# Optimization experiments

Hardware: AMD Instinct MI355X
Metric: run time of the kernel (lower is better)

## Reference

```python
import jax, jax.numpy as jnp
import numpy as np

N_NODES = 50000
BN_EPS = 1e-5


def setup_inputs() -> dict:
    key = jax.random.key(0)
    ks = jax.random.split(key, 16)
    N, IN, H, OUT, E = N_NODES, 512, 128, 64, 800000
    s = lambda fi, fo: 1.0 / np.sqrt(fi)
    inp = {
        'x': jax.random.normal(ks[0], (N, IN), dtype=jnp.float32),
        'edge_index': jax.random.randint(ks[1], (2, E), 0, N, dtype=jnp.int32),
        # mlpA: Linear(N -> H)
        'WA': jax.random.uniform(ks[2], (H, N), jnp.float32, -s(N, H), s(N, H)),
        'bA': jax.random.uniform(ks[3], (H,), jnp.float32, -s(N, H), s(N, H)),
        # mlpX: Linear(IN -> H)
        'WX': jax.random.uniform(ks[4], (H, IN), jnp.float32, -s(IN, H), s(IN, H)),
        'bX': jax.random.uniform(ks[5], (H,), jnp.float32, -s(IN, H), s(IN, H)),
        # W: Linear(2H -> H)
        'W': jax.random.uniform(ks[6], (H, 2 * H), jnp.float32, -s(2 * H, H), s(2 * H, H)),
        'bW': jax.random.uniform(ks[7], (H,), jnp.float32, -s(2 * H, H), s(2 * H, H)),
        # mlp_final layer 1: Linear(H -> H) + BN
        'Wf1': jax.random.uniform(ks[8], (H, H), jnp.float32, -s(H, H), s(H, H)),
        'bf1': jax.random.uniform(ks[9], (H,), jnp.float32, -s(H, H), s(H, H)),
        'gamma': jnp.ones((H,), jnp.float32),
        'beta': jnp.zeros((H,), jnp.float32),
        # mlp_final layer 2: Linear(H -> OUT)
        'Wf2': jax.random.uniform(ks[10], (OUT, H), jnp.float32, -s(H, OUT), s(H, OUT)),
        'bf2': jax.random.uniform(ks[11], (OUT,), jnp.float32, -s(H, OUT), s(H, OUT)),
    }
    return inp


def _batchnorm(x, gamma, beta):
    # training-mode BN over the node/batch axis (biased variance, as in torch)
    mean = jnp.mean(x, axis=0)
    var = jnp.var(x, axis=0)
    return (x - mean) * jax.lax.rsqrt(var + BN_EPS) * gamma + beta


def reference(x, edge_index, WA, bA, WX, bX, W, bW, Wf1, bf1, gamma, beta, Wf2, bf2):
    row, col = edge_index[0], edge_index[1]
    row = row - row.min()
    # xA = A @ WA.T + bA  where A[i,j]=1 per (row,col) edge (duplicates sum).
    # Equivalent SpMM: gather columns of WA at `col`, segment-sum into `row`.
    xA = jax.ops.segment_sum(WA.T[col], row, num_segments=N_NODES) + bA  # [N, H]
    xX = x @ WX.T + bX  # [N, H]
    h = jnp.concatenate([xA, xX], axis=-1) @ W.T + bW  # [N, H]
    h = jax.nn.relu(h + xA + xX)
    # mlp_final (num_layers=2): Linear -> ReLU -> BN -> (dropout off) -> Linear
    h = jax.nn.relu(h @ Wf1.T + bf1)
    h = _batchnorm(h, gamma, beta)
    out = h @ Wf2.T + bf2  # [N, OUT]
    return out
```

## Files before the change

### kernel.cpp

```cpp
#include <hip/hip_runtime.h>

typedef __bf16 bf16_t;
typedef __bf16 bf16x8 __attribute__((ext_vector_type(8)));
typedef float f32x4 __attribute__((ext_vector_type(4)));

#define IN_DIM 512
#define H_DIM 128
#define OUT_DIM 64
#define BN_EPS 1e-5f
#define SCAN_BLK 2048

#define MFMA(a, b, c) __builtin_amdgcn_mfma_f32_16x16x32_bf16(a, b, c, 0, 0, 0)

__device__ __forceinline__ float ld_adapt(const void* p, size_t i, int isbf) {
    return isbf ? (float)((const bf16_t*)p)[i] : ((const float*)p)[i];
}

__device__ __forceinline__ void split8(const float* p, bf16x8& hi, bf16x8& lo) {
    f32x4 v0 = *(const f32x4*)p;
    f32x4 v1 = *(const f32x4*)(p + 4);
#pragma unroll
    for (int i = 0; i < 8; ++i) {
        float f = (i < 4) ? v0[i] : v1[i - 4];
        bf16_t h = (bf16_t)f;
        hi[i] = h;
        lo[i] = (bf16_t)(f - (float)h);
    }
}

__device__ __forceinline__ void loadAraw(const void* x, size_t elemoff, int isbf,
                                         f32x4& p0, f32x4& p1) {
    if (isbf) {
        p0 = *(const f32x4*)((const bf16_t*)x + elemoff);
    } else {
        const float* fp = (const float*)x + elemoff;
        p0 = *(const f32x4*)fp;
        p1 = *(const f32x4*)(fp + 4);
    }
}

__device__ __forceinline__ void cvtA(const f32x4& p0, const f32x4& p1, int isbf,
                                     bf16x8& ah, bf16x8& al) {
    if (isbf) {
        ah = __builtin_bit_cast(bf16x8, p0);
#pragma unroll
        for (int i = 0; i < 8; ++i) al[i] = (bf16_t)0.f;
    } else {
#pragma unroll
        for (int i = 0; i < 8; ++i) {
            float f = (i < 4) ? p0[i] : p1[i - 4];
            bf16_t h = (bf16_t)f;
            ah[i] = h;
            al[i] = (bf16_t)(f - (float)h);
        }
    }
}

__global__ void k_init(const void* bA, const void* bX, const void* bW, const void* bf1,
                       const void* gamma, const void* beta, const void* bf2,
                       float* __restrict__ dst, int* __restrict__ flag) {
    __shared__ int s_isbf;
    if (threadIdx.x == 0) {
        unsigned u = *(const unsigned*)gamma;
        int f = (u == 0x3F803F80u) ? 1 : 0;
        *flag = f;
        s_isbf = f;
    }
    __syncthreads();
    int isbf = s_isbf;
    int t = threadIdx.x;
    dst[t] = ld_adapt(bA, t, isbf);
    dst[128 + t] = ld_adapt(bX, t, isbf);
    dst[256 + t] = ld_adapt(bW, t, isbf);
    dst[384 + t] = ld_adapt(bf1, t, isbf);
    dst[512 + t] = ld_adapt(gamma, t, isbf);
    dst[640 + t] = ld_adapt(beta, t, isbf);
    if (t < OUT_DIM) dst[768 + t] = ld_adapt(bf2, t, isbf);
}

__global__ __launch_bounds__(256) void k_transpose(const void* __restrict__ WA,
                                                   float* __restrict__ WAT, int N,
                                                   const int* __restrict__ flag) {
    __shared__ float t[64][130];
    int isbf = *flag;
    int n0 = blockIdx.x * 64;
    int tid = threadIdx.x;
#pragma unroll
    for (int i = 0; i < 32; ++i) {
        int lin = i * 256 + tid;
        int h = lin >> 6, nl = lin & 63;
        int n = n0 + nl;
        t[nl][h] = (n < N) ? ld_adapt(WA, (size_t)h * N + n, isbf) : 0.f;
    }
    __syncthreads();
#pragma unroll
    for (int i = 0; i < 32; ++i) {
        int lin = i * 256 + tid;
        int nl = lin >> 7, h = lin & 127;
        int n = n0 + nl;
        if (n < N) WAT[(size_t)n * H_DIM + h] = t[nl][h];
    }
}

__global__ __launch_bounds__(256) void k_prep(const int* __restrict__ rows, int E,
                                              int* __restrict__ bmin, int* __restrict__ cnt) {
    __shared__ int sm[4];
    int i = blockIdx.x * 256 + threadIdx.x;
    int m = 0x7fffffff;
    if (i < E) {
        int r = rows[i];
        m = r;
        atomicAdd(&cnt[r], 1);
    }
    for (int off = 32; off; off >>= 1) m = min(m, __shfl_xor(m, off, 64));
    if ((threadIdx.x & 63) == 0) sm[threadIdx.x >> 6] = m;
    __syncthreads();
    if (threadIdx.x == 0)
        bmin[blockIdx.x] = min(min(sm[0], sm[1]), min(sm[2], sm[3]));
}

__global__ __launch_bounds__(256) void k_scan1(const int* __restrict__ cnt,
                                               int* __restrict__ offs,
                                               int* __restrict__ bsum, int N) {
    __shared__ int ts[256];
    int base = blockIdx.x * SCAN_BLK;
    int t = threadIdx.x;
    int v[8], s = 0;
#pragma unroll
    for (int i = 0; i < 8; ++i) {
        int idx = base + t * 8 + i;
        v[i] = (idx < N) ? cnt[idx] : 0;
        s += v[i];
    }
    ts[t] = s;
    __syncthreads();
    for (int off = 1; off < 256; off <<= 1) {
        int x = (t >= off) ? ts[t - off] : 0;
        __syncthreads();
        ts[t] += x;
        __syncthreads();
    }
    int run = ts[t] - s;
#pragma unroll
    for (int i = 0; i < 8; ++i) {
        int idx = base + t * 8 + i;
        if (idx < N) offs[idx] = run;
        run += v[i];
    }
    if (t == 255) bsum[blockIdx.x] = ts[255];
}

__global__ __launch_bounds__(256) void k_scan2(int* __restrict__ bsum, int* __restrict__ offs,
                                               int NB, int N, const int* __restrict__ bmin,
                                               int nbmin, int* __restrict__ minbuf) {
    __shared__ int sm[256];
    int t = threadIdx.x;
    int m = 0x7fffffff;
    for (int i = t; i < nbmin; i += 256) m = min(m, bmin[i]);
    sm[t] = m;
    __syncthreads();
    for (int off = 128; off; off >>= 1) {
        if (t < off) sm[t] = min(sm[t], sm[t + off]);
        __syncthreads();
    }
    if (t == 0) {
        *minbuf = sm[0];
        int run = 0;
        for (int b = 0; b < NB; ++b) {
            int v = bsum[b];
            bsum[b] = run;
            run += v;
        }
        offs[N] = run;
    }
}

__global__ __launch_bounds__(256) void k_scan3(int* __restrict__ offs, const int* __restrict__ bsum,
                                               int* __restrict__ cursor, int N) {
    int i = blockIdx.x * 256 + threadIdx.x;
    if (i >= N) return;
    int v = offs[i] + bsum[i / SCAN_BLK];
    offs[i] = v;
    cursor[i] = v;
}

__global__ __launch_bounds__(256) void k_build(const int* __restrict__ rows,
                                               const int* __restrict__ cols, int E,
                                               int* __restrict__ cursor,
                                               int* __restrict__ scol) {
    int i = blockIdx.x * 256 + threadIdx.x;
    if (i >= E) return;
    int r = rows[i];
    int pos = atomicAdd(&cursor[r], 1);
    scol[pos] = cols[i];
}

__global__ __launch_bounds__(256) void k_gather(const int* __restrict__ offs,
                                                const int* __restrict__ scol,
                                                const float* __restrict__ WAT,
                                                const float* __restrict__ bA_f,
                                                const int* __restrict__ minbuf,
                                                float* __restrict__ xA, int N) {
    int wave = threadIdx.x >> 6, lane = threadIdx.x & 63;
    int r = blockIdx.x * 4 + wave;
    if (r >= N) return;
    int b = r + *minbuf;
    int s = 0, e = 0;
    if (b < N) {
        s = offs[b];
        e = offs[b + 1];
    }
    float2 a0 = {0.f, 0.f}, a1 = {0.f, 0.f}, a2 = {0.f, 0.f}, a3 = {0.f, 0.f};
    int i = s;
    for (; i + 7 < e; i += 8) {
        float2 w[8];
#pragma unroll
        for (int j = 0; j < 8; ++j) {
            int c = scol[i + j];
            w[j] = *(const float2*)(WAT + (size_t)c * H_DIM + lane * 2);
        }
        a0.x += w[0].x + w[4].x; a0.y += w[0].y + w[4].y;
        a1.x += w[1].x + w[5].x; a1.y += w[1].y + w[5].y;
        a2.x += w[2].x + w[6].x; a2.y += w[2].y + w[6].y;
        a3.x += w[3].x + w[7].x; a3.y += w[3].y + w[7].y;
    }
    for (; i + 1 < e; i += 2) {
        int c0 = scol[i], c1 = scol[i + 1];
        float2 w0 = *(const float2*)(WAT + (size_t)c0 * H_DIM + lane * 2);
        float2 w1 = *(const float2*)(WAT + (size_t)c1 * H_DIM + lane * 2);
        a0.x += w0.x; a0.y += w0.y;
        a1.x += w1.x; a1.y += w1.y;
    }
    if (i < e) {
        int c = scol[i];
        float2 w = *(const float2*)(WAT + (size_t)c * H_DIM + lane * 2);
        a2.x += w.x; a2.y += w.y;
    }
    float2 bias = *(const float2*)(bA_f + lane * 2);
    float2 out = {a0.x + a1.x + a2.x + a3.x + bias.x, a0.y + a1.y + a2.y + a3.y + bias.y};
    *(float2*)(xA + (size_t)r * H_DIM + lane * 2) = out;
}

__device__ __forceinline__ void pack_frag(const void* __restrict__ W, bf16_t* __restrict__ hi,
                                          bf16_t* __restrict__ lo, int K, int NC,
                                          int addres, int isbf, int f, int lane) {
    int ks = f / (NC >> 4), nt = f % (NC >> 4);
    int n = nt * 16 + (lane & 15);
    int k0 = ks * 32 + (lane >> 4) * 8;
    bf16_t* dh = hi + (size_t)f * 512 + lane * 8;
    bf16_t* dl = lo + (size_t)f * 512 + lane * 8;
#pragma unroll
    for (int j = 0; j < 8; ++j) {
        int kk = k0 + j;
        float v = ld_adapt(W, (size_t)n * K + kk, isbf);
        if (addres && (kk == n || kk == n + H_DIM)) v += 1.f;
        bf16_t h = (bf16_t)v;
        dh[j] = h;
        dl[j] = (bf16_t)(v - (float)h);
    }
}

__global__ __launch_bounds__(256) void k_pack3(const void* WX, bf16_t* WXh, bf16_t* WXl,
                                               const void* W, bf16_t* Wh, bf16_t* Wl,
                                               const void* Wf1, bf16_t* Wf1h, bf16_t* Wf1l,
                                               const int* __restrict__ flag) {
    int g = blockIdx.x * 256 + threadIdx.x;
    int f = g >> 6, lane = g & 63;
    int isbf = *flag;
    if (f < 128)
        pack_frag(WX, WXh, WXl, IN_DIM, H_DIM, 0, isbf, f, lane);
    else if (f < 192)
        pack_frag(W, Wh, Wl, 2 * H_DIM, H_DIM, 1, isbf, f - 128, lane);
    else if (f < 224)
        pack_frag(Wf1, Wf1h, Wf1l, H_DIM, H_DIM, 0, isbf, f - 192, lane);
}

__global__ __launch_bounds__(256, 2) void k_fuseA(
    const void* __restrict__ x, const float* __restrict__ xAf,
    const bf16_t* __restrict__ WXh, const bf16_t* __restrict__ WXl,
    const bf16_t* __restrict__ Wh, const bf16_t* __restrict__ Wl,
    const bf16_t* __restrict__ Wf1h, const bf16_t* __restrict__ Wf1l,
    const float* __restrict__ smallf, float* __restrict__ h2,
    double* __restrict__ sums, double* __restrict__ sumsq,
    const int* __restrict__ flag, int M) {
    __shared__ float ax[32 * 132];
    __shared__ float ls_sum[H_DIM], ls_sq[H_DIM];
    int tid = threadIdx.x;
    int wave = tid >> 6, lane = tid & 63, l16 = lane & 15, quad = lane >> 4;
    int band = wave & 1, half = wave >> 1;
    int ntb = half * 4;
    int mbase = blockIdx.x * 32 + band * 16;
    int isbf = *flag;
    int r0 = min(mbase + l16, M - 1);
    const float* bX = smallf + 128;
    const float* bW = smallf + 256;
    const float* bf1 = smallf + 384;

    if (tid < H_DIM) {
        ls_sum[tid] = 0.f;
        ls_sq[tid] = 0.f;
    }

    auto loadB = [&](const bf16_t* __restrict__ H, const bf16_t* __restrict__ L, int fb,
                     bf16x8 bh[4], bf16x8 bl[4]) {
        const bf16_t* hp = H + (size_t)fb * 512 + lane * 8;
        const bf16_t* lp = L + (size_t)fb * 512 + lane * 8;
#pragma unroll
        for (int nt = 0; nt < 4; ++nt) {
            bh[nt] = *(const bf16x8*)(hp + nt * 512);
            bl[nt] = *(const bf16x8*)(lp + nt * 512);
        }
    };

    f32x4 acc[4];
    bf16x8 bh[2][4], bl[2][4];
    f32x4 pa[2][2];

#pragma unroll
    for (int nt = 0; nt < 4; ++nt) acc[nt] = f32x4{0.f, 0.f, 0.f, 0.f};
    {
        size_t offx = (size_t)r0 * IN_DIM + quad * 8;
        loadAraw(x, offx, isbf, pa[0][0], pa[0][1]);
        loadB(WXh, WXl, ntb, bh[0], bl[0]);
#pragma unroll
        for (int ks = 0; ks < 16; ++ks) {
            int cur = ks & 1, nxt = cur ^ 1;
            if (ks < 15) {
                loadAraw(x, offx + (ks + 1) * 32, isbf, pa[nxt][0], pa[nxt][1]);
                loadB(WXh, WXl, (ks + 1) * 8 + ntb, bh[nxt], bl[nxt]);
            }
            bf16x8 ah, al;
            cvtA(pa[cur][0], pa[cur][1], isbf, ah, al);
#pragma unroll
            for (int nt = 0; nt < 4; ++nt) {
                acc[nt] = MFMA(ah, bh[cur][nt], acc[nt]);
                acc[nt] = MFMA(ah, bl[cur][nt], acc[nt]);
                acc[nt] = MFMA(al, bh[cur][nt], acc[nt]);
            }
        }
    }
#pragma unroll
    for (int nt = 0; nt < 4; ++nt) {
        int col = (ntb + nt) * 16 + l16;
        float b = bX[col];
#pragma unroll
        for (int r = 0; r < 4; ++r) {
            int lr = band * 16 + quad * 4 + r;
            ax[lr * 132 + col] = acc[nt][r] + b;
        }
    }
    __syncthreads();

#pragma unroll
    for (int nt = 0; nt < 4; ++nt) acc[nt] = f32x4{0.f, 0.f, 0.f, 0.f};
    {
        size_t aoff = (size_t)r0 * H_DIM + quad * 8;
        const float* axp = ax + (band * 16 + l16) * 132 + quad * 8;
        pa[0][0] = *(const f32x4*)(xAf + aoff);
        pa[0][1] = *(const f32x4*)(xAf + aoff + 4);
        loadB(Wh, Wl, ntb, bh[0], bl[0]);
#pragma unroll
        for (int ks = 0; ks < 8; ++ks) {
            int cur = ks & 1, nxt = cur ^ 1;
            if (ks < 7) loadB(Wh, Wl, (ks + 1) * 8 + ntb, bh[nxt], bl[nxt]);
            if (ks < 3) {
                pa[nxt][0] = *(const f32x4*)(xAf + aoff + (ks + 1) * 32);
                pa[nxt][1] = *(const f32x4*)(xAf + aoff + (ks + 1) * 32 + 4);
            }
            bf16x8 ah, al;
            if (ks < 4)
                cvtA(pa[cur][0], pa[cur][1], 0, ah, al);
            else
                split8(axp + (ks - 4) * 32, ah, al);
#pragma unroll
            for (int nt = 0; nt < 4; ++nt) {
                acc[nt] = MFMA(ah, bh[cur][nt], acc[nt]);
                acc[nt] = MFMA(ah, bl[cur][nt], acc[nt]);
                acc[nt] = MFMA(al, bh[cur][nt], acc[nt]);
            }
        }
    }
    __syncthreads();
#pragma unroll
    for (int nt = 0; nt < 4; ++nt) {
        int col = (ntb + nt) * 16 + l16;
        float b = bW[col];
#pragma unroll
        for (int r = 0; r < 4; ++r) {
            int lr = band * 16 + quad * 4 + r;
            ax[lr * 132 + col] = fmaxf(acc[nt][r] + b, 0.f);
        }
    }
    __syncthreads();

#pragma unroll
    for (int nt = 0; nt < 4; ++nt) acc[nt] = f32x4{0.f, 0.f, 0.f, 0.f};
    {
        const float* axp = ax + (band * 16 + l16) * 132 + quad * 8;
        loadB(Wf1h, Wf1l, ntb, bh[0], bl[0]);
#pragma unroll
        for (int ks = 0; ks < 4; ++ks) {
            int cur = ks & 1, nxt = cur ^ 1;
            if (ks < 3) loadB(Wf1h, Wf1l, (ks + 1) * 8 + ntb, bh[nxt], bl[nxt]);
            bf16x8 ah, al;
            split8(axp + ks * 32, ah, al);
#pragma unroll
            for (int nt = 0; nt < 4; ++nt) {
                acc[nt] = MFMA(ah, bh[cur][nt], acc[nt]);
                acc[nt] = MFMA(ah, bl[cur][nt], acc[nt]);
                acc[nt] = MFMA(al, bh[cur][nt], acc[nt]);
            }
        }
    }
#pragma unroll
    for (int nt = 0; nt < 4; ++nt) {
        int col = (ntb + nt) * 16 + l16;
        float b = bf1[col];
        float s = 0.f, s2 = 0.f;
#pragma unroll
        for (int r = 0; r < 4; ++r) {
            int row = mbase + quad * 4 + r;
            if (row < M) {
                float v = fmaxf(acc[nt][r] + b, 0.f);
                h2[(size_t)row * H_DIM + col] = v;
                s += v;
                s2 += v * v;
            }
        }
        s += __shfl_xor(s, 16, 64);
        s += __shfl_xor(s, 32, 64);
        s2 += __shfl_xor(s2, 16, 64);
        s2 += __shfl_xor(s2, 32, 64);
        if (quad == 0) {
            atomicAdd(&ls_sum[col], s);
            atomicAdd(&ls_sq[col], s2);
        }
    }
    __syncthreads();
    if (tid < H_DIM) {
        atomicAdd(&sums[tid], (double)ls_sum[tid]);
        atomicAdd(&sumsq[tid], (double)ls_sq[tid]);
    }
}

__global__ __launch_bounds__(256) void k_fuseB(
    const float* __restrict__ h2, const void* __restrict__ Wf2,
    const float* __restrict__ smallf, const double* __restrict__ sums,
    const double* __restrict__ sumsq, void* __restrict__ outv,
    const int* __restrict__ flag, int M) {
    __shared__ bf16_t wh[16 * 512];
    __shared__ bf16_t wl[16 * 512];
    __shared__ float aw[H_DIM], cw[H_DIM], b2[OUT_DIM];
    int t = threadIdx.x;
    int isbf = *flag;
    const float* gamma_f = smallf + 512;
    const float* beta_f = smallf + 640;
    const float* bf2_f = smallf + 768;

    if (t < H_DIM) {
        double mean = sums[t] / (double)M;
        double var = sumsq[t] / (double)M - mean * mean;
        if (var < 0) var = 0;
        float a = gamma_f[t] * rsqrtf((float)var + BN_EPS);
        aw[t] = a;
        cw[t] = beta_f[t] - (float)mean * a;
    }
    __syncthreads();
    if (t < OUT_DIM) {
        float acc = bf2_f[t];
        for (int j = 0; j < H_DIM; ++j) acc += ld_adapt(Wf2, (size_t)t * H_DIM + j, isbf) * cw[j];
        b2[t] = acc;
    }
    for (int u = t; u < 1024; u += 256) {
        int f = u >> 6, ln = u & 63;
        int ks = f >> 2, nt = f & 3;
        int n = nt * 16 + (ln & 15);
        int k0 = ks * 32 + (ln >> 4) * 8;
#pragma unroll
        for (int j = 0; j < 8; ++j) {
            float v = ld_adapt(Wf2, (size_t)n * H_DIM + k0 + j, isbf) * aw[k0 + j];
            bf16_t h = (bf16_t)v;
            wh[f * 512 + ln * 8 + j] = h;
            wl[f * 512 + ln * 8 + j] = (bf16_t)(v - (float)h);
        }
    }
    __syncthreads();

    int wave = t >> 6, lane = t & 63, l16 = lane & 15, quad = lane >> 4;
    int mbase = blockIdx.x * 64 + wave * 16;
    int r0 = min(mbase + l16, M - 1);
    f32x4 acc4[4];
#pragma unroll
    for (int nt = 0; nt < 4; ++nt) acc4[nt] = f32x4{0.f, 0.f, 0.f, 0.f};
    for (int ks = 0; ks < 4; ++ks) {
        bf16x8 ah, al;
        split8(h2 + (size_t)r0 * H_DIM + ks * 32 + quad * 8, ah, al);
#pragma unroll
        for (int nt = 0; nt < 4; ++nt) {
            bf16x8 bh = *(const bf16x8*)(wh + (ks * 4 + nt) * 512 + lane * 8);
            bf16x8 bl = *(const bf16x8*)(wl + (ks * 4 + nt) * 512 + lane * 8);
            acc4[nt] = MFMA(ah, bh, acc4[nt]);
            acc4[nt] = MFMA(ah, bl, acc4[nt]);
            acc4[nt] = MFMA(al, bh, acc4[nt]);
        }
    }
#pragma unroll
    for (int nt = 0; nt < 4; ++nt) {
        int col = nt * 16 + l16;
        float b = b2[col];
#pragma unroll
        for (int r = 0; r < 4; ++r) {
            int row = mbase + quad * 4 + r;
            if (row < M) {
                float v = acc4[nt][r] + b;
                if (isbf)
                    ((bf16_t*)outv)[(size_t)row * OUT_DIM + col] = (bf16_t)v;
                else
                    ((float*)outv)[(size_t)row * OUT_DIM + col] = v;
            }
        }
    }
}

extern "C" void kernel_launch(void* const* d_in, const int* in_sizes, int n_in,
                              void* d_out, int out_size, void* d_ws, size_t ws_size,
                              hipStream_t stream) {
    const void* x = d_in[0];
    const int* ei = (const int*)d_in[1];
    const void* WA = d_in[2];
    const void* bA = d_in[3];
    const void* WX = d_in[4];
    const void* bX = d_in[5];
    const void* W = d_in[6];
    const void* bW = d_in[7];
    const void* Wf1 = d_in[8];
    const void* bf1 = d_in[9];
    const void* gamma = d_in[10];
    const void* beta = d_in[11];
    const void* Wf2 = d_in[12];
    const void* bf2 = d_in[13];

    const int N = in_sizes[0] / IN_DIM;
    const int E = in_sizes[1] / 2;
    const int* rows = ei;
    const int* cols = ei + E;
    const int eblocks = (E + 255) / 256;

    char* ws = (char*)d_ws;
    size_t off = 0;
    auto alloc = [&](size_t bytes) {
        char* p = ws + off;
        off += (bytes + 255) & ~(size_t)255;
        return p;
    };
    int* flag = (int*)alloc(4);
    int* minbuf = (int*)alloc(4);
    float* smallf = (float*)alloc(832 * 4);
    double* sums = (double*)alloc(2 * H_DIM * 8);
    double* sumsq = sums + H_DIM;
    bf16_t* WXp_h = (bf16_t*)alloc((size_t)IN_DIM * H_DIM * 2);
    bf16_t* WXp_l = (bf16_t*)alloc((size_t)IN_DIM * H_DIM * 2);
    bf16_t* Wp_h = (bf16_t*)alloc((size_t)256 * H_DIM * 2);
    bf16_t* Wp_l = (bf16_t*)alloc((size_t)256 * H_DIM * 2);
    bf16_t* Wf1p_h = (bf16_t*)alloc((size_t)H_DIM * H_DIM * 2);
    bf16_t* Wf1p_l = (bf16_t*)alloc((size_t)H_DIM * H_DIM * 2);
    int* cnt = (int*)alloc((size_t)N * 4);
    int* offs = (int*)alloc(((size_t)N + 1) * 4);
    int* cursor = (int*)alloc((size_t)N * 4);
    int* bsum = (int*)alloc(64 * 4);
    int* bmin = (int*)alloc((size_t)eblocks * 4);
    int* scol = (int*)alloc((size_t)E * 4);
    float* WAT = (float*)alloc((size_t)N * H_DIM * 4);
    float* xAf = (float*)alloc((size_t)N * H_DIM * 4);
    float* h2 = WAT;

    float* bA_f = smallf + 0;

    hipMemsetAsync(cnt, 0, (size_t)N * 4, stream);
    hipMemsetAsync(sums, 0, 2 * H_DIM * 8, stream);

    k_init<<<1, 128, 0, stream>>>(bA, bX, bW, bf1, gamma, beta, bf2, smallf, flag);
    k_transpose<<<(N + 63) / 64, 256, 0, stream>>>(WA, WAT, N, flag);
    k_pack3<<<56, 256, 0, stream>>>(WX, WXp_h, WXp_l, W, Wp_h, Wp_l, Wf1, Wf1p_h, Wf1p_l, flag);

    k_prep<<<eblocks, 256, 0, stream>>>(rows, E, bmin, cnt);
    int NB = (N + SCAN_BLK - 1) / SCAN_BLK;
    k_scan1<<<NB, 256, 0, stream>>>(cnt, offs, bsum, N);
    k_scan2<<<1, 256, 0, stream>>>(bsum, offs, NB, N, bmin, eblocks, minbuf);
    k_scan3<<<(N + 255) / 256, 256, 0, stream>>>(offs, bsum, cursor, N);
    k_build<<<eblocks, 256, 0, stream>>>(rows, cols, E, cursor, scol);
    k_gather<<<(N + 3) / 4, 256, 0, stream>>>(offs, scol, WAT, bA_f, minbuf, xAf, N);

    k_fuseA<<<(N + 31) / 32, 256, 0, stream>>>(x, xAf, WXp_h, WXp_l, Wp_h, Wp_l, Wf1p_h, Wf1p_l,
                                               smallf, h2, sums, sumsq, flag, N);
    k_fuseB<<<(N + 63) / 64, 256, 0, stream>>>(h2, Wf2, smallf, sums, sumsq, d_out, flag, N);
}
```

Measured before the change: 503.5 us.

## Specialize bf16 input path: bf16 WAT table, drop lo-part MFMAs, remove init kernel

Removes the k_init kernel and the stored flag by detecting bf16 inputs inline from gamma in every kernel, and reads biases directly. When inputs are bf16, the transposed WA table is stored as bf16 to halve gather traffic. k_fuseA is templated on precision so the bf16 path skips the low-part weight loads and extra MFMAs, and the fp32 path drops software prefetching of the lo weights and launch_bounds occupancy hint. The fp32 default path may lose some pipelining in the first GEMM, while the bf16 path accepts reduced precision from the bf16 WAT.

```diff
diff --git a/kernel.cpp b/kernel.cpp
--- a/kernel.cpp
+++ b/kernel.cpp
@@ -2,6 +2,7 @@
 
 typedef __bf16 bf16_t;
 typedef __bf16 bf16x8 __attribute__((ext_vector_type(8)));
+typedef __bf16 bf16x2 __attribute__((ext_vector_type(2)));
 typedef float f32x4 __attribute__((ext_vector_type(4)));
 
 #define IN_DIM 512
@@ -12,6 +13,10 @@
 
 #define MFMA(a, b, c) __builtin_amdgcn_mfma_f32_16x16x32_bf16(a, b, c, 0, 0, 0)
 
+__device__ __forceinline__ int detect_bf(const void* gamma) {
+    return (*(const unsigned*)gamma == 0x3F803F80u) ? 1 : 0;
+}
+
 __device__ __forceinline__ float ld_adapt(const void* p, size_t i, int isbf) {
     return isbf ? (float)((const bf16_t*)p)[i] : ((const float*)p)[i];
 }
@@ -28,61 +33,11 @@
     }
 }
 
-__device__ __forceinline__ void loadAraw(const void* x, size_t elemoff, int isbf,
-                                         f32x4& p0, f32x4& p1) {
-    if (isbf) {
-        p0 = *(const f32x4*)((const bf16_t*)x + elemoff);
-    } else {
-        const float* fp = (const float*)x + elemoff;
-        p0 = *(const f32x4*)fp;
-        p1 = *(const f32x4*)(fp + 4);
-    }
-}
-
-__device__ __forceinline__ void cvtA(const f32x4& p0, const f32x4& p1, int isbf,
-                                     bf16x8& ah, bf16x8& al) {
-    if (isbf) {
-        ah = __builtin_bit_cast(bf16x8, p0);
-#pragma unroll
-        for (int i = 0; i < 8; ++i) al[i] = (bf16_t)0.f;
-    } else {
-#pragma unroll
-        for (int i = 0; i < 8; ++i) {
-            float f = (i < 4) ? p0[i] : p1[i - 4];
-            bf16_t h = (bf16_t)f;
-            ah[i] = h;
-            al[i] = (bf16_t)(f - (float)h);
-        }
-    }
-}
-
-__global__ void k_init(const void* bA, const void* bX, const void* bW, const void* bf1,
-                       const void* gamma, const void* beta, const void* bf2,
-                       float* __restrict__ dst, int* __restrict__ flag) {
-    __shared__ int s_isbf;
-    if (threadIdx.x == 0) {
-        unsigned u = *(const unsigned*)gamma;
-        int f = (u == 0x3F803F80u) ? 1 : 0;
-        *flag = f;
-        s_isbf = f;
-    }
-    __syncthreads();
-    int isbf = s_isbf;
-    int t = threadIdx.x;
-    dst[t] = ld_adapt(bA, t, isbf);
-    dst[128 + t] = ld_adapt(bX, t, isbf);
-    dst[256 + t] = ld_adapt(bW, t, isbf);
-    dst[384 + t] = ld_adapt(bf1, t, isbf);
-    dst[512 + t] = ld_adapt(gamma, t, isbf);
-    dst[640 + t] = ld_adapt(beta, t, isbf);
-    if (t < OUT_DIM) dst[768 + t] = ld_adapt(bf2, t, isbf);
-}
-
 __global__ __launch_bounds__(256) void k_transpose(const void* __restrict__ WA,
-                                                   float* __restrict__ WAT, int N,
-                                                   const int* __restrict__ flag) {
+                                                   void* __restrict__ WAT, int N,
+                                                   const void* __restrict__ gamma) {
     __shared__ float t[64][130];
-    int isbf = *flag;
+    int isbf = detect_bf(gamma);
     int n0 = blockIdx.x * 64;
     int tid = threadIdx.x;
 #pragma unroll
@@ -98,7 +53,13 @@
         int lin = i * 256 + tid;
         int nl = lin >> 7, h = lin & 127;
         int n = n0 + nl;
-        if (n < N) WAT[(size_t)n * H_DIM + h] = t[nl][h];
+        if (n < N) {
+            float v = t[nl][h];
+            if (isbf)
+                ((bf16_t*)WAT)[(size_t)n * H_DIM + h] = (bf16_t)v;
+            else
+                ((float*)WAT)[(size_t)n * H_DIM + h] = v;
+        }
     }
 }
 
@@ -197,10 +158,12 @@
 
 __global__ __launch_bounds__(256) void k_gather(const int* __restrict__ offs,
                                                 const int* __restrict__ scol,
-                                                const float* __restrict__ WAT,
-                                                const float* __restrict__ bA_f,
+                                                const void* __restrict__ WAT,
+                                                const void* __restrict__ bA,
                                                 const int* __restrict__ minbuf,
-                                                float* __restrict__ xA, int N) {
+                                                float* __restrict__ xA, int N,
+                                                const void* __restrict__ gamma) {
+    int isbf = detect_bf(gamma);
     int wave = threadIdx.x >> 6, lane = threadIdx.x & 63;
     int r = blockIdx.x * 4 + wave;
     if (r >= N) return;
@@ -212,32 +175,48 @@
     }
     float2 a0 = {0.f, 0.f}, a1 = {0.f, 0.f}, a2 = {0.f, 0.f}, a3 = {0.f, 0.f};
     int i = s;
-    for (; i + 7 < e; i += 8) {
-        float2 w[8];
-#pragma unroll
-        for (int j = 0; j < 8; ++j) {
-            int c = scol[i + j];
-            w[j] = *(const float2*)(WAT + (size_t)c * H_DIM + lane * 2);
-        }
-        a0.x += w[0].x + w[4].x; a0.y += w[0].y + w[4].y;
-        a1.x += w[1].x + w[5].x; a1.y += w[1].y + w[5].y;
-        a2.x += w[2].x + w[6].x; a2.y += w[2].y + w[6].y;
-        a3.x += w[3].x + w[7].x; a3.y += w[3].y + w[7].y;
-    }
-    for (; i + 1 < e; i += 2) {
-        int c0 = scol[i], c1 = scol[i + 1];
-        float2 w0 = *(const float2*)(WAT + (size_t)c0 * H_DIM + lane * 2);
-        float2 w1 = *(const float2*)(WAT + (size_t)c1 * H_DIM + lane * 2);
-        a0.x += w0.x; a0.y += w0.y;
-        a1.x += w1.x; a1.y += w1.y;
-    }
-    if (i < e) {
-        int c = scol[i];
-        float2 w = *(const float2*)(WAT + (size_t)c * H_DIM + lane * 2);
-        a2.x += w.x; a2.y += w.y;
-    }
-    float2 bias = *(const float2*)(bA_f + lane * 2);
-    float2 out = {a0.x + a1.x + a2.x + a3.x + bias.x, a0.y + a1.y + a2.y + a3.y + bias.y};
+    if (isbf) {
+        const bf16_t* Wb = (const bf16_t*)WAT;
+        for (; i + 7 < e; i += 8) {
+            bf16x2 w[8];
+#pragma unroll
+            for (int j = 0; j < 8; ++j) {
+                int c = scol[i + j];
+                w[j] = *(const bf16x2*)(Wb + (size_t)c * H_DIM + lane * 2);
+            }
+            a0.x += (float)w[0][0] + (float)w[4][0]; a0.y += (float)w[0][1] + (float)w[4][1];
+            a1.x += (float)w[1][0] + (float)w[5][0]; a1.y += (float)w[1][1] + (float)w[5][1];
+            a2.x += (float)w[2][0] + (float)w[6][0]; a2.y += (float)w[2][1] + (float)w[6][1];
+            a3.x += (float)w[3][0] + (float)w[7][0]; a3.y += (float)w[3][1] + (float)w[7][1];
+        }
+        for (; i < e; ++i) {
+            int c = scol[i];
+            bf16x2 w = *(const bf16x2*)(Wb + (size_t)c * H_DIM + lane * 2);
+            a0.x += (float)w[0]; a0.y += (float)w[1];
+        }
+    } else {
+        const float* Wf = (const float*)WAT;
+        for (; i + 7 < e; i += 8) {
+            float2 w[8];
+#pragma unroll
+            for (int j = 0; j < 8; ++j) {
+                int c = scol[i + j];
+                w[j] = *(const float2*)(Wf + (size_t)c * H_DIM + lane * 2);
+            }
+            a0.x += w[0].x + w[4].x; a0.y += w[0].y + w[4].y;
+            a1.x += w[1].x + w[5].x; a1.y += w[1].y + w[5].y;
+            a2.x += w[2].x + w[6].x; a2.y += w[2].y + w[6].y;
+            a3.x += w[3].x + w[7].x; a3.y += w[3].y + w[7].y;
+        }
+        for (; i < e; ++i) {
+            int c = scol[i];
+            float2 w = *(const float2*)(Wf + (size_t)c * H_DIM + lane * 2);
+            a0.x += w.x; a0.y += w.y;
+        }
+    }
+    float bx = ld_adapt(bA, lane * 2, isbf);
+    float by = ld_adapt(bA, lane * 2 + 1, isbf);
+    float2 out = {a0.x + a1.x + a2.x + a3.x + bx, a0.y + a1.y + a2.y + a3.y + by};
     *(float2*)(xA + (size_t)r * H_DIM + lane * 2) = out;
 }
 
@@ -263,10 +242,10 @@
 __global__ __launch_bounds__(256) void k_pack3(const void* WX, bf16_t* WXh, bf16_t* WXl,
                                                const void* W, bf16_t* Wh, bf16_t* Wl,
                                                const void* Wf1, bf16_t* Wf1h, bf16_t* Wf1l,
-                                               const int* __restrict__ flag) {
+                                               const void* __restrict__ gamma) {
     int g = blockIdx.x * 256 + threadIdx.x;
     int f = g >> 6, lane = g & 63;
-    int isbf = *flag;
+    int isbf = detect_bf(gamma);
     if (f < 128)
         pack_frag(WX, WXh, WXl, IN_DIM, H_DIM, 0, isbf, f, lane);
     else if (f < 192)
@@ -275,74 +254,72 @@
         pack_frag(Wf1, Wf1h, Wf1l, H_DIM, H_DIM, 0, isbf, f - 192, lane);
 }
 
-__global__ __launch_bounds__(256, 2) void k_fuseA(
+template <int ISBF>
+__device__ __forceinline__ void fuseA_body(
     const void* __restrict__ x, const float* __restrict__ xAf,
     const bf16_t* __restrict__ WXh, const bf16_t* __restrict__ WXl,
     const bf16_t* __restrict__ Wh, const bf16_t* __restrict__ Wl,
     const bf16_t* __restrict__ Wf1h, const bf16_t* __restrict__ Wf1l,
-    const float* __restrict__ smallf, float* __restrict__ h2,
-    double* __restrict__ sums, double* __restrict__ sumsq,
-    const int* __restrict__ flag, int M) {
-    __shared__ float ax[32 * 132];
-    __shared__ float ls_sum[H_DIM], ls_sq[H_DIM];
+    const void* __restrict__ bX, const void* __restrict__ bWv, const void* __restrict__ bf1,
+    float* __restrict__ h2, double* __restrict__ sums, double* __restrict__ sumsq,
+    float* ax, float* ls_sum, float* ls_sq, int M) {
     int tid = threadIdx.x;
     int wave = tid >> 6, lane = tid & 63, l16 = lane & 15, quad = lane >> 4;
     int band = wave & 1, half = wave >> 1;
     int ntb = half * 4;
     int mbase = blockIdx.x * 32 + band * 16;
-    int isbf = *flag;
     int r0 = min(mbase + l16, M - 1);
-    const float* bX = smallf + 128;
-    const float* bW = smallf + 256;
-    const float* bf1 = smallf + 384;
 
     if (tid < H_DIM) {
         ls_sum[tid] = 0.f;
         ls_sq[tid] = 0.f;
     }
 
-    auto loadB = [&](const bf16_t* __restrict__ H, const bf16_t* __restrict__ L, int fb,
-                     bf16x8 bh[4], bf16x8 bl[4]) {
+    f32x4 acc[4];
+    bf16x8 bh[2][4], bl4[4];
+
+    auto loadB4 = [&](const bf16_t* __restrict__ H, int fb, bf16x8 dst[4]) {
         const bf16_t* hp = H + (size_t)fb * 512 + lane * 8;
-        const bf16_t* lp = L + (size_t)fb * 512 + lane * 8;
-#pragma unroll
-        for (int nt = 0; nt < 4; ++nt) {
-            bh[nt] = *(const bf16x8*)(hp + nt * 512);
-            bl[nt] = *(const bf16x8*)(lp + nt * 512);
-        }
+#pragma unroll
+        for (int nt = 0; nt < 4; ++nt) dst[nt] = *(const bf16x8*)(hp + nt * 512);
     };
 
-    f32x4 acc[4];
-    bf16x8 bh[2][4], bl[2][4];
-    f32x4 pa[2][2];
-
 #pragma unroll
     for (int nt = 0; nt < 4; ++nt) acc[nt] = f32x4{0.f, 0.f, 0.f, 0.f};
-    {
-        size_t offx = (size_t)r0 * IN_DIM + quad * 8;
-        loadAraw(x, offx, isbf, pa[0][0], pa[0][1]);
-        loadB(WXh, WXl, ntb, bh[0], bl[0]);
+    if (ISBF) {
+        const bf16_t* xb = (const bf16_t*)x + (size_t)r0 * IN_DIM + quad * 8;
+        bf16x8 a[2];
+        a[0] = *(const bf16x8*)xb;
+        loadB4(WXh, ntb, bh[0]);
 #pragma unroll
         for (int ks = 0; ks < 16; ++ks) {
             int cur = ks & 1, nxt = cur ^ 1;
             if (ks < 15) {
-                loadAraw(x, offx + (ks + 1) * 32, isbf, pa[nxt][0], pa[nxt][1]);
-                loadB(WXh, WXl, (ks + 1) * 8 + ntb, bh[nxt], bl[nxt]);
-            }
+                a[nxt] = *(const bf16x8*)(xb + (ks + 1) * 32);
+                loadB4(WXh, (ks + 1) * 8 + ntb, bh[nxt]);
+            }
+#pragma unroll
+            for (int nt = 0; nt < 4; ++nt) acc[nt] = MFMA(a[cur], bh[cur][nt], acc[nt]);
+        }
+    } else {
+        const float* xf = (const float*)x + (size_t)r0 * IN_DIM + quad * 8;
+        for (int ks = 0; ks < 16; ++ks) {
             bf16x8 ah, al;
-            cvtA(pa[cur][0], pa[cur][1], isbf, ah, al);
+            split8(xf + ks * 32, ah, al);
+            loadB4(WXh, ks * 8 + ntb, bh[0]);
+            loadB4(WXl, ks * 8 + ntb, bl4);
 #pragma unroll
             for (int nt = 0; nt < 4; ++nt) {
-                acc[nt] = MFMA(ah, bh[cur][nt], acc[nt]);
-                acc[nt] = MFMA(ah, bl[cur][nt], acc[nt]);
-                acc[nt] = MFMA(al, bh[cur][nt], acc[nt]);
+                acc[nt] = MFMA(ah, bh[0][nt], acc[nt]);
+                acc[nt] = MFMA(ah, bl4[nt], acc[nt]);
+                acc[nt] = MFMA(al, bh[0][nt], acc[nt]);
             }
         }
     }
 #pragma unroll
     for (int nt = 0; nt < 4; ++nt) {
         int col = (ntb + nt) * 16 + l16;
-        float b = bX[col];
+        float b = ld_adapt(bX, col, ISBF);
 #pragma unroll
         for (int r = 0; r < 4; ++r) {
             int lr = band * 16 + quad * 4 + r;
@@ -356,27 +333,36 @@
     {
         size_t aoff = (size_t)r0 * H_DIM + quad * 8;
         const float* axp = ax + (band * 16 + l16) * 132 + quad * 8;
+        f32x4 pa[2][2];
         pa[0][0] = *(const f32x4*)(xAf + aoff);
         pa[0][1] = *(const f32x4*)(xAf + aoff + 4);
-        loadB(Wh, Wl, ntb, bh[0], bl[0]);
+        loadB4(Wh, ntb, bh[0]);
 #pragma unroll
         for (int ks = 0; ks < 8; ++ks) {
             int cur = ks & 1, nxt = cur ^ 1;
-            if (ks < 7) loadB(Wh, Wl, (ks + 1) * 8 + ntb, bh[nxt], bl[nxt]);
+            if (ks < 7) loadB4(Wh, (ks + 1) * 8 + ntb, bh[nxt]);
             if (ks < 3) {
                 pa[nxt][0] = *(const f32x4*)(xAf + aoff + (ks + 1) * 32);
                 pa[nxt][1] = *(const f32x4*)(xAf + aoff + (ks + 1) * 32 + 4);
             }
             bf16x8 ah, al;
-            if (ks < 4)
-                cvtA(pa[cur][0], pa[cur][1], 0, ah, al);
-            else
+            if (ks < 4) {
+#pragma unroll
+                for (int i = 0; i < 8; ++i) {
+                    float f = (i < 4) ? pa[cur][0][i] : pa[cur][1][i - 4];
+                    bf16_t h = (bf16_t)f;
+                    ah[i] = h;
+                    al[i] = (bf16_t)(f - (float)h);
+                }
+            } else {
                 split8(axp + (ks - 4) * 32, ah, al);
+            }
+            if (!ISBF) loadB4(Wl, ks * 8 + ntb, bl4);
 #pragma unroll
             for (int nt = 0; nt < 4; ++nt) {
                 acc[nt] = MFMA(ah, bh[cur][nt], acc[nt]);
-                acc[nt] = MFMA(ah, bl[cur][nt], acc[nt]);
                 acc[nt] = MFMA(al, bh[cur][nt], acc[nt]);
+                if (!ISBF) acc[nt] = MFMA(ah, bl4[nt], acc[nt]);
             }
         }
     }
@@ -384,7 +370,7 @@
 #pragma unroll
     for (int nt = 0; nt < 4; ++nt) {
         int col = (ntb + nt) * 16 + l16;
-        float b = bW[col];
+        float b = ld_adapt(bWv, col, ISBF);
 #pragma unroll
         for (int r = 0; r < 4; ++r) {
             int lr = band * 16 + quad * 4 + r;
@@ -397,25 +383,26 @@
     for (int nt = 0; nt < 4; ++nt) acc[nt] = f32x4{0.f, 0.f, 0.f, 0.f};
     {
         const float* axp = ax + (band * 16 + l16) * 132 + quad * 8;
-        loadB(Wf1h, Wf1l, ntb, bh[0], bl[0]);
+        loadB4(Wf1h, ntb, bh[0]);
 #pragma unroll
         for (int ks = 0; ks < 4; ++ks) {
             int cur = ks & 1, nxt = cur ^ 1;
-            if (ks < 3) loadB(Wf1h, Wf1l, (ks + 1) * 8 + ntb, bh[nxt], bl[nxt]);
+            if (ks < 3) loadB4(Wf1h, (ks + 1) * 8 + ntb, bh[nxt]);
             bf16x8 ah, al;
             split8(axp + ks * 32, ah, al);
+            if (!ISBF) loadB4(Wf1l, ks * 8 + ntb, bl4);
 #pragma unroll
             for (int nt = 0; nt < 4; ++nt) {
                 acc[nt] = MFMA(ah, bh[cur][nt], acc[nt]);
-                acc[nt] = MFMA(ah, bl[cur][nt], acc[nt]);
                 acc[nt] = MFMA(al, bh[cur][nt], acc[nt]);
+                if (!ISBF) acc[nt] = MFMA(ah, bl4[nt], acc[nt]);
             }
         }
     }
 #pragma unroll
     for (int nt = 0; nt < 4; ++nt) {
         int col = (ntb + nt) * 16 + l16;
-        float b = bf1[col];
+        float b = ld_adapt(bf1, col, ISBF);
         float s = 0.f, s2 = 0.f;
 #pragma unroll
         for (int r = 0; r < 4; ++r) {
@@ -443,31 +430,46 @@
     }
 }
 
+__global__ __launch_bounds__(256) void k_fuseA(
+    const void* __restrict__ x, const float* __restrict__ xAf,
+    const bf16_t* __restrict__ WXh, const bf16_t* __restrict__ WXl,
+    const bf16_t* __restrict__ Wh, const bf16_t* __restrict__ Wl,
+    const bf16_t* __restrict__ Wf1h, const bf16_t* __restrict__ Wf1l,
+    const void* __restrict__ bX, const void* __restrict__ bWv, const void* __restrict__ bf1,
+    float* __restrict__ h2, double* __restrict__ sums, double* __restrict__ sumsq,
+    const void* __restrict__ gamma, int M) {
+    __shared__ float ax[32 * 132];
+    __shared__ float ls_sum[H_DIM], ls_sq[H_DIM];
+    if (detect_bf(gamma))
+        fuseA_body<1>(x, xAf, WXh, WXl, Wh, Wl, Wf1h, Wf1l, bX, bWv, bf1, h2, sums, sumsq,
+                      ax, ls_sum, ls_sq, M);
+    else
+        fuseA_body<0>(x, xAf, WXh, WXl, Wh, Wl, Wf1h, Wf1l, bX, bWv, bf1, h2, sums, sumsq,
+                      ax, ls_sum, ls_sq, M);
+}
+
 __global__ __launch_bounds__(256) void k_fuseB(
     const float* __restrict__ h2, const void* __restrict__ Wf2,
-    const float* __restrict__ smallf, const double* __restrict__ sums,
-    const double* __restrict__ sumsq, void* __restrict__ outv,
-    const int* __restrict__ flag, int M) {
+    const void* __restrict__ gamma, const void* __restrict__ beta, const void* __restrict__ bf2,
+    const double* __restrict__ sums, const double* __restrict__ sumsq,
+    void* __restrict__ outv, int M) {
     __shared__ bf16_t wh[16 * 512];
     __shared__ bf16_t wl[16 * 512];
     __shared__ float aw[H_DIM], cw[H_DIM], b2[OUT_DIM];
     int t = threadIdx.x;
-    int isbf = *flag;
-    const float* gamma_f = smallf + 512;
-    const float* beta_f = smallf + 640;
-    const float* bf2_f = smallf + 768;
+    int isbf = detect_bf(gamma);
 
     if (t < H_DIM) {
         double mean = sums[t] / (double)M;
         double var = sumsq[t] / (double)M - mean * mean;
         if (var < 0) var = 0;
-        float a = gamma_f[t] * rsqrtf((float)var + BN_EPS);
+        float a = ld_adapt(gamma, t, isbf) * rsqrtf((float)var + BN_EPS);
         aw[t] = a;
-        cw[t] = beta_f[t] - (float)mean * a;
+        cw[t] = ld_adapt(beta, t, isbf) - (float)mean * a;
     }
     __syncthreads();
     if (t < OUT_DIM) {
-        float acc = bf2_f[t];
+        float acc = ld_adapt(bf2, t, isbf);
         for (int j = 0; j < H_DIM; ++j) acc += ld_adapt(Wf2, (size_t)t * H_DIM + j, isbf) * cw[j];
         b2[t] = acc;
     }
@@ -553,9 +555,7 @@
         off += (bytes + 255) & ~(size_t)255;
         return p;
     };
-    int* flag = (int*)alloc(4);
     int* minbuf = (int*)alloc(4);
-    float* smallf = (float*)alloc(832 * 4);
     double* sums = (double*)alloc(2 * H_DIM * 8);
     double* sumsq = sums + H_DIM;
     bf16_t* WXp_h = (bf16_t*)alloc((size_t)IN_DIM * H_DIM * 2);
@@ -570,18 +570,15 @@
     int* bsum = (int*)alloc(64 * 4);
     int* bmin = (int*)alloc((size_t)eblocks * 4);
     int* scol = (int*)alloc((size_t)E * 4);
-    float* WAT = (float*)alloc((size_t)N * H_DIM * 4);
+    void* WAT = (void*)alloc((size_t)N * H_DIM * 4);
     float* xAf = (float*)alloc((size_t)N * H_DIM * 4);
-    float* h2 = WAT;
-
-    float* bA_f = smallf + 0;
+    float* h2 = (float*)WAT;
 
     hipMemsetAsync(cnt, 0, (size_t)N * 4, stream);
     hipMemsetAsync(sums, 0, 2 * H_DIM * 8, stream);
 
-    k_init<<<1, 128, 0, stream>>>(bA, bX, bW, bf1, gamma, beta, bf2, smallf, flag);
-    k_transpose<<<(N + 63) / 64, 256, 0, stream>>>(WA, WAT, N, flag);
-    k_pack3<<<56, 256, 0, stream>>>(WX, WXp_h, WXp_l, W, Wp_h, Wp_l, Wf1, Wf1p_h, Wf1p_l, flag);
+    k_transpose<<<(N + 63) / 64, 256, 0, stream>>>(WA, WAT, N, gamma);
+    k_pack3<<<56, 256, 0, stream>>>(WX, WXp_h, WXp_l, W, Wp_h, Wp_l, Wf1, Wf1p_h, Wf1p_l, gamma);
 
     k_prep<<<eblocks, 256, 0, stream>>>(rows, E, bmin, cnt);
     int NB = (N + SCAN_BLK - 1) / SCAN_BLK;
@@ -589,9 +586,9 @@
     k_scan2<<<1, 256, 0, stream>>>(bsum, offs, NB, N, bmin, eblocks, minbuf);
     k_scan3<<<(N + 255) / 256, 256, 0, stream>>>(offs, bsum, cursor, N);
     k_build<<<eblocks, 256, 0, stream>>>(rows, cols, E, cursor, scol);
-    k_gather<<<(N + 3) / 4, 256, 0, stream>>>(offs, scol, WAT, bA_f, minbuf, xAf, N);
+    k_gather<<<(N + 3) / 4, 256, 0, stream>>>(offs, scol, WAT, bA, minbuf, xAf, N, gamma);
 
     k_fuseA<<<(N + 31) / 32, 256, 0, stream>>>(x, xAf, WXp_h, WXp_l, Wp_h, Wp_l, Wf1p_h, Wf1p_l,
-                                               smallf, h2, sums, sumsq, flag, N);
-    k_fuseB<<<(N + 63) / 64, 256, 0, stream>>>(h2, Wf2, smallf, sums, sumsq, d_out, flag, N);
-}
+                                               bX, bW, bf1, h2, sums, sumsq, gamma, N);
+    k_fuseB<<<(N + 63) / 64, 256, 0, stream>>>(h2, Wf2, gamma, beta, bf2, sums, sumsq, d_out, N);
+}
```

Result: faster. 491.7 us (-2.3%).
